# Optimization experiments

Measured on AMD Instinct MI355X. Metric: run time of the kernel, lower is better.

## Reference

```python
import jax, jax.numpy as jnp
import numpy as np

B, NQ, NKV, D, H = 8, 1024, 2048, 1024, 16
HD = D // H
EPS = 1e-5  # torch F.layer_norm default


def make_rope(n, hd):
    # standard RoPE tables: theta=10000, freqs repeated to head_dim via half/half layout
    inv = 1.0 / (10000.0 ** (np.arange(0, hd, 2, dtype=np.float64) / hd))
    ang = np.arange(n, dtype=np.float64)[:, None] * inv[None, :]  # [n, hd/2]
    ang = np.concatenate([ang, ang], axis=-1)  # [n, hd]
    return jnp.asarray(np.cos(ang), jnp.float32), jnp.asarray(np.sin(ang), jnp.float32)


def setup_inputs() -> dict:
    key = jax.random.key(0)
    ks = jax.random.split(key, 8)
    s = 1.0 / np.sqrt(D)
    q_cos, q_sin = make_rope(NQ, HD)
    kv_cos, kv_sin = make_rope(NKV, HD)
    return {
        "q_in": jax.random.normal(ks[0], (B, NQ, D), jnp.float32),
        "kv_in": jax.random.normal(ks[1], (B, NKV, D), jnp.float32),
        "q_cos": q_cos, "q_sin": q_sin,
        "kv_cos": kv_cos, "kv_sin": kv_sin,
        "Wq": jax.random.normal(ks[2], (D, D), jnp.float32) * s,
        "bq": jnp.zeros((D,), jnp.float32),
        "Wk": jax.random.normal(ks[3], (D, D), jnp.float32) * s,
        "bk": jnp.zeros((D,), jnp.float32),
        "Wv": jax.random.normal(ks[4], (D, D), jnp.float32) * s,
        "bv": jnp.zeros((D,), jnp.float32),
        "Wo": jax.random.normal(ks[5], (D, D), jnp.float32) * s,
        "bo": jnp.zeros((D,), jnp.float32),
    }


def _layer_norm(x):
    mu = jnp.mean(x, axis=-1, keepdims=True)
    var = jnp.mean(jnp.square(x - mu), axis=-1, keepdims=True)
    return (x - mu) * jax.lax.rsqrt(var + EPS)


def _to_multihead(x):
    # [B, N, D] -> [B, H, N, hd]
    b, n, _ = x.shape
    return x.reshape(b, n, H, HD).transpose(0, 2, 1, 3)


def _rotate_half(x):
    x1, x2 = jnp.split(x, 2, axis=-1)
    return jnp.concatenate([-x2, x1], axis=-1)


def _rope(x, cos, sin):
    # x: [B, H, N, hd]; cos/sin: [N, hd]
    return x * cos[None, None] + _rotate_half(x) * sin[None, None]


def reference(q_in, kv_in, q_cos, q_sin, kv_cos, kv_sin,
              Wq, bq, Wk, bk, Wv, bv, Wo, bo):
    qn = _layer_norm(q_in)
    kvn = _layer_norm(kv_in)
    q = _to_multihead(qn @ Wq.T + bq)
    k = _to_multihead(kvn @ Wk.T + bk)
    v = _to_multihead(kvn @ Wv.T + bv)
    q = _rope(q, q_cos, q_sin)
    k = _rope(k, kv_cos, kv_sin)
    # SDPA
    scores = jnp.einsum('bhqd,bhkd->bhqk', q, k) / np.sqrt(HD).astype(np.float32)
    attn = jax.nn.softmax(scores, axis=-1)
    out = jnp.einsum('bhqk,bhkd->bhqd', attn, v)  # [B, H, NQ, hd]
    out = out.transpose(0, 2, 1, 3).reshape(q_in.shape[0], q_in.shape[1], D)
    return out @ Wo.T + bo
```

## Files before the change

### kernel.cpp

```cpp
#include <hip/hip_runtime.h>
#include <stdint.h>
#include <stddef.h>

#define B_   8
#define NQ_  1024
#define NKV_ 2048
#define D_   1024
#define H_   16
#define HD_  64

typedef __bf16 bf16;
typedef __bf16 bf16x4 __attribute__((ext_vector_type(4)));
typedef __bf16 bf16x8 __attribute__((ext_vector_type(8)));
typedef float  f32x2  __attribute__((ext_vector_type(2)));
typedef float  f32x4  __attribute__((ext_vector_type(4)));
typedef float  f32x16 __attribute__((ext_vector_type(16)));
typedef unsigned int u32;
typedef u32 u32x2 __attribute__((ext_vector_type(2)));
typedef u32 u32x4 __attribute__((ext_vector_type(4)));
typedef unsigned short u16;

__device__ __forceinline__ void gload_lds16(const void* g, void* l) {
  __builtin_amdgcn_global_load_lds((const __attribute__((address_space(1))) void*)g,
                                   (__attribute__((address_space(3))) void*)l, 16, 0, 0);
}

__device__ __forceinline__ u32 pack2(float a, float b) {
  u16 ua = __builtin_bit_cast(u16, (bf16)a);
  u16 ub = __builtin_bit_cast(u16, (bf16)b);
  return (u32)ua | ((u32)ub << 16);
}

__global__ void cvt_w_kernel(const float* __restrict__ w0, const float* __restrict__ w1,
                             const float* __restrict__ w2, const float* __restrict__ w3,
                             bf16* __restrict__ o0, bf16* __restrict__ o1,
                             bf16* __restrict__ o2, bf16* __restrict__ o3) {
  const float* s; bf16* d;
  switch (blockIdx.y) {
    case 0: s = w0; d = o0; break;
    case 1: s = w1; d = o1; break;
    case 2: s = w2; d = o2; break;
    default: s = w3; d = o3; break;
  }
  int i = (blockIdx.x * 256 + threadIdx.x) * 4;
  float4 v = *(const float4*)(s + i);
  bf16x4 t = { (bf16)v.x, (bf16)v.y, (bf16)v.z, (bf16)v.w };
  *(bf16x4*)(d + i) = t;
}

__global__ void ln_bf16_kernel(const float* __restrict__ x, bf16* __restrict__ y) {
  int w = threadIdx.x >> 6, l = threadIdx.x & 63;
  int row = blockIdx.x * 4 + w;
  const float* xr = x + (size_t)row * D_;
  float4 v[4];
#pragma unroll
  for (int k = 0; k < 4; ++k) v[k] = *(const float4*)(xr + k * 256 + l * 4);
  float s = 0.f, ss = 0.f;
#pragma unroll
  for (int k = 0; k < 4; ++k) {
    s  += v[k].x + v[k].y + v[k].z + v[k].w;
    ss += v[k].x * v[k].x + v[k].y * v[k].y + v[k].z * v[k].z + v[k].w * v[k].w;
  }
#pragma unroll
  for (int m = 1; m < 64; m <<= 1) { s += __shfl_xor(s, m); ss += __shfl_xor(ss, m); }
  float mu = s * (1.f / D_);
  float var = ss * (1.f / D_) - mu * mu;
  float rs = rsqrtf(var + 1e-5f);
  bf16* yr = y + (size_t)row * D_;
#pragma unroll
  for (int k = 0; k < 4; ++k) {
    bf16x4 t = { (bf16)((v[k].x - mu) * rs), (bf16)((v[k].y - mu) * rs),
                 (bf16)((v[k].z - mu) * rs), (bf16)((v[k].w - mu) * rs) };
    *(bf16x4*)(yr + k * 256 + l * 4) = t;
  }
}

__device__ __forceinline__ int swz64(int row, int slot) {
  return row * 64 + ((slot ^ ((row >> 1) & 3)) << 4);
}

template<int EPI>
__global__ __launch_bounds__(256)
void gemm_bt(const bf16* __restrict__ A, const bf16* __restrict__ Bw,
             const float* __restrict__ bias,
             const float* __restrict__ cosT, const float* __restrict__ sinT,
             void* __restrict__ outp, int seq_shift) {
  __shared__ bf16 As[2][128 * 32];
  __shared__ bf16 Bs[2][128 * 32];
  const int tid = threadIdx.x;
  const int w = tid >> 6, l = tid & 63;
  const int wr = w >> 1, wc = w & 1;
  const int lg = l >> 4, lr = l & 15;
  const int mbase = blockIdx.y * 128, nbase = blockIdx.x * 128;

  f32x4 acc[4][4] = {};

  auto stage = [&](int k0, int buf) {
#pragma unroll
    for (int i = 0; i < 2; ++i) {
      int S = i * 256 + tid;
      int row = S >> 2, st = S & 3;
      int gs = st ^ ((row >> 1) & 3);
      gload_lds16((const char*)(A + ((size_t)(mbase + row) * 1024 + k0)) + gs * 16,
                  (char*)&As[buf][0] + (i * 256 + w * 64) * 16);
    }
#pragma unroll
    for (int i = 0; i < 2; ++i) {
      int S = i * 256 + tid;
      int row = S >> 2, st = S & 3;
      int gs = st ^ ((row >> 1) & 3);
      gload_lds16((const char*)(Bw + ((size_t)(nbase + row) * 1024 + k0)) + gs * 16,
                  (char*)&Bs[buf][0] + (i * 256 + w * 64) * 16);
    }
  };

  stage(0, 0);
  __syncthreads();
  for (int it = 0; it < 32; ++it) {
    int buf = it & 1;
    if (it + 1 < 32) stage((it + 1) * 32, buf ^ 1);
    bf16x8 af[4], bfr[4];
#pragma unroll
    for (int fr = 0; fr < 4; ++fr)
      af[fr] = *(const bf16x8*)((const char*)&As[buf][0] + swz64(wr * 64 + fr * 16 + lr, lg));
#pragma unroll
    for (int fc = 0; fc < 4; ++fc)
      bfr[fc] = *(const bf16x8*)((const char*)&Bs[buf][0] + swz64(wc * 64 + fc * 16 + lr, lg));
#pragma unroll
    for (int fr = 0; fr < 4; ++fr)
#pragma unroll
      for (int fc = 0; fc < 4; ++fc)
        acc[fr][fc] = __builtin_amdgcn_mfma_f32_16x16x32_bf16(af[fr], bfr[fc], acc[fr][fc], 0, 0, 0);
    __syncthreads();
  }

#pragma unroll
  for (int fr = 0; fr < 4; ++fr)
#pragma unroll
    for (int r = 0; r < 4; ++r) {
      int mrow = mbase + wr * 64 + fr * 16 + lg * 4 + r;
#pragma unroll
      for (int fc = 0; fc < 4; ++fc) {
        int n = nbase + wc * 64 + fc * 16 + lr;
        float x = acc[fr][fc][r];
        if (EPI == 0) {
          float xb  = x + bias[n];
          float xpb = acc[fr][fc ^ 2][r] + bias[n ^ 32];
          int d = n & 63, h = n >> 6;
          int seqN = 1 << seq_shift;
          int pos = mrow & (seqN - 1), bi = mrow >> seq_shift;
          float c = cosT[pos * 64 + d], s2 = sinT[pos * 64 + d];
          float yv = xb * c + ((d < 32) ? -xpb : xpb) * s2;
          ((bf16*)outp)[((size_t)(bi * H_ + h) * seqN + pos) * 64 + d] = (bf16)yv;
        } else if (EPI == 2) {
          int bi = n >> 11, kp = n & (NKV_ - 1);
          ((bf16*)outp)[(size_t)bi * (1024 * NKV_) + (size_t)mrow * NKV_ + kp] =
              (bf16)(x + bias[mrow]);
        } else {
          ((float*)outp)[(size_t)mrow * 1024 + n] = x + bias[n];
        }
      }
    }
}

__device__ __forceinline__ int swz128(int row, int slot) {
  return row * 128 + ((slot ^ (row & 7)) << 4);
}

__global__ __launch_bounds__(256)
void attn_kernel(const bf16* __restrict__ Qh, const bf16* __restrict__ Kh,
                 const bf16* __restrict__ Vt, bf16* __restrict__ Ao) {
  __shared__ bf16 Ks[2][64 * 64];
  __shared__ bf16 Vs[2][64 * 64];
  const int tid = threadIdx.x, wq = tid >> 6, l = tid & 63;
  const int q31 = l & 31, h = l >> 5;

  int bid = blockIdx.x;
  int vid = (bid & 7) * 128 + (bid >> 3);
  const int bh = vid >> 3;
  const int q0 = (vid & 7) * 128;

  bf16x8 aq[4];
  {
    const bf16* qrow = Qh + ((size_t)bh * NQ_ + q0 + wq * 32 + q31) * 64;
#pragma unroll
    for (int kt = 0; kt < 4; ++kt) aq[kt] = *(const bf16x8*)(qrow + kt * 16 + h * 8);
  }

  const char* Kbase = (const char*)(Kh + (size_t)bh * NKV_ * 64);
  const char* Vbase = (const char*)(Vt + (size_t)bh * 64 * NKV_);

  auto stageKV = [&](int t, int buf) {
#pragma unroll
    for (int i = 0; i < 2; ++i) {
      int S = i * 256 + tid;
      int row = S >> 3, st = S & 7;
      int gs = st ^ (row & 7);
      gload_lds16(Kbase + (size_t)(t * 64 + row) * 128 + gs * 16,
                  (char*)&Ks[buf][0] + (i * 256 + wq * 64) * 16);
    }
#pragma unroll
    for (int i = 0; i < 2; ++i) {
      int S = i * 256 + tid;
      int row = S >> 3, st = S & 7;
      int gs = st ^ (row & 7);
      gload_lds16(Vbase + (size_t)row * (NKV_ * 2) + (size_t)t * 128 + gs * 16,
                  (char*)&Vs[buf][0] + (i * 256 + wq * 64) * 16);
    }
  };

  float mrun = -3.0e38f, lrun = 0.f;
  f32x16 oaccT[2] = {};

  stageKV(0, 0);
  __syncthreads();

  const float SC = 0.125f * 1.44269504f;

  for (int t = 0; t < NKV_ / 64; ++t) {
    int buf = t & 1;
    if (t + 1 < NKV_ / 64) stageKV(t + 1, buf ^ 1);

    f32x16 st[2] = {};
    __builtin_amdgcn_s_setprio(1);
#pragma unroll
    for (int kvt = 0; kvt < 2; ++kvt)
#pragma unroll
      for (int kt = 0; kt < 4; ++kt) {
        bf16x8 kf = *(const bf16x8*)((const char*)&Ks[buf][0] +
                                     swz128(kvt * 32 + q31, kt * 2 + h));
        st[kvt] = __builtin_amdgcn_mfma_f32_32x32x16_bf16(kf, aq[kt], st[kvt], 0, 0, 0);
      }
    __builtin_amdgcn_s_setprio(0);

    f32x2 m2 = { -3.0e38f, -3.0e38f };
#pragma unroll
    for (int kvt = 0; kvt < 2; ++kvt)
#pragma unroll
      for (int i = 0; i < 8; ++i) {
        f32x2 v = { st[kvt][2 * i], st[kvt][2 * i + 1] };
        m2 = __builtin_elementwise_max(m2, v);
      }
    float ms = fmaxf(m2.x, m2.y);
    ms = fmaxf(ms, __shfl_xor(ms, 32));

    if (!__all((ms - mrun) * SC <= 8.0f)) {
      float mn = fmaxf(mrun, ms);
      float alpha = exp2f((mrun - mn) * SC);
      mrun = mn;
      lrun *= alpha;
#pragma unroll
      for (int dt = 0; dt < 2; ++dt) oaccT[dt] *= alpha;
    }
    float bterm = mrun * SC;

    f32x2 rs2 = { 0.f, 0.f };
    const f32x2 sc2 = { SC, SC };
    const f32x2 nb2 = { -bterm, -bterm };
#pragma unroll
    for (int kvt = 0; kvt < 2; ++kvt)
#pragma unroll
      for (int i = 0; i < 8; ++i) {
        f32x2 v = { st[kvt][2 * i], st[kvt][2 * i + 1] };
        v = v * sc2 + nb2;
        f32x2 p = { exp2f(v.x), exp2f(v.y) };
        st[kvt][2 * i] = p.x;
        st[kvt][2 * i + 1] = p.y;
        rs2 = rs2 + p;
      }
    float rs = rs2.x + rs2.y;
    rs += __shfl_xor(rs, 32);
    lrun += rs;

    bf16x8 pf[4];
#pragma unroll
    for (int kvt = 0; kvt < 2; ++kvt) {
      u32 E0 = pack2(st[kvt][0],  st[kvt][1]);
      u32 E1 = pack2(st[kvt][2],  st[kvt][3]);
      u32 O0 = pack2(st[kvt][4],  st[kvt][5]);
      u32 O1 = pack2(st[kvt][6],  st[kvt][7]);
      u32 E2 = pack2(st[kvt][8],  st[kvt][9]);
      u32 E3 = pack2(st[kvt][10], st[kvt][11]);
      u32 O2 = pack2(st[kvt][12], st[kvt][13]);
      u32 O3 = pack2(st[kvt][14], st[kvt][15]);
      u32 r0 = (u32)__shfl_xor((int)(h ? E0 : O0), 32);
      u32 r1 = (u32)__shfl_xor((int)(h ? E1 : O1), 32);
      u32 r2 = (u32)__shfl_xor((int)(h ? E2 : O2), 32);
      u32 r3 = (u32)__shfl_xor((int)(h ? E3 : O3), 32);
      u32x4 f0 = { h ? r0 : E0, h ? r1 : E1, h ? O0 : r0, h ? O1 : r1 };
      u32x4 f1 = { h ? r2 : E2, h ? r3 : E3, h ? O2 : r2, h ? O3 : r3 };
      pf[kvt * 2 + 0] = __builtin_bit_cast(bf16x8, f0);
      pf[kvt * 2 + 1] = __builtin_bit_cast(bf16x8, f1);
    }

    __builtin_amdgcn_s_setprio(1);
#pragma unroll
    for (int dt = 0; dt < 2; ++dt)
#pragma unroll
      for (int vt = 0; vt < 4; ++vt) {
        bf16x8 av = *(const bf16x8*)((const char*)&Vs[buf][0] +
                                     swz128(dt * 32 + q31, vt * 2 + h));
        oaccT[dt] = __builtin_amdgcn_mfma_f32_32x32x16_bf16(av, pf[vt], oaccT[dt], 0, 0, 0);
      }
    __builtin_amdgcn_s_setprio(0);
    __syncthreads();
  }

  float inv = 1.f / lrun;
  int b = bh >> 4, hh = bh & 15;
  bf16* orow = Ao + ((size_t)b * NQ_ + q0 + wq * 32 + q31) * D_ + hh * 64;
#pragma unroll
  for (int dt = 0; dt < 2; ++dt)
#pragma unroll
    for (int g = 0; g < 4; ++g) {
      int d = dt * 32 + 8 * g + 4 * h;
      u32 p0 = pack2(oaccT[dt][g * 4 + 0] * inv, oaccT[dt][g * 4 + 1] * inv);
      u32 p1 = pack2(oaccT[dt][g * 4 + 2] * inv, oaccT[dt][g * 4 + 3] * inv);
      *(u32*)(orow + d) = p0;
      *(u32*)(orow + d + 2) = p1;
    }
}

extern "C" void kernel_launch(void* const* d_in, const int* in_sizes, int n_in,
                              void* d_out, int out_size, void* d_ws, size_t ws_size,
                              hipStream_t stream) {
  (void)in_sizes; (void)n_in; (void)out_size; (void)ws_size;
  const float* q_in   = (const float*)d_in[0];
  const float* kv_in  = (const float*)d_in[1];
  const float* q_cos  = (const float*)d_in[2];
  const float* q_sin  = (const float*)d_in[3];
  const float* kv_cos = (const float*)d_in[4];
  const float* kv_sin = (const float*)d_in[5];
  const float* Wq = (const float*)d_in[6];
  const float* bq = (const float*)d_in[7];
  const float* Wk = (const float*)d_in[8];
  const float* bk = (const float*)d_in[9];
  const float* Wv = (const float*)d_in[10];
  const float* bv = (const float*)d_in[11];
  const float* Wo = (const float*)d_in[12];
  const float* bo = (const float*)d_in[13];

  char* ws = (char*)d_ws;
  bf16* qn  = (bf16*)ws;              ws += (size_t)B_ * NQ_ * D_ * 2;
  bf16* kvn = (bf16*)ws;              ws += (size_t)B_ * NKV_ * D_ * 2;
  bf16* wqb = (bf16*)ws;              ws += (size_t)D_ * D_ * 2;
  bf16* wkb = (bf16*)ws;              ws += (size_t)D_ * D_ * 2;
  bf16* wvb = (bf16*)ws;              ws += (size_t)D_ * D_ * 2;
  bf16* wob = (bf16*)ws;              ws += (size_t)D_ * D_ * 2;
  bf16* Qh  = (bf16*)ws;              ws += (size_t)B_ * H_ * NQ_ * 64 * 2;
  bf16* Kh  = (bf16*)ws;              ws += (size_t)B_ * H_ * NKV_ * 64 * 2;
  bf16* Vt  = (bf16*)ws;              ws += (size_t)B_ * H_ * 64 * NKV_ * 2;
  bf16* Ao  = qn;

  cvt_w_kernel<<<dim3(1024, 4), 256, 0, stream>>>(Wq, Wk, Wv, Wo, wqb, wkb, wvb, wob);
  ln_bf16_kernel<<<(B_ * NQ_) / 4, 256, 0, stream>>>(q_in, qn);
  ln_bf16_kernel<<<(B_ * NKV_) / 4, 256, 0, stream>>>(kv_in, kvn);

  gemm_bt<0><<<dim3(D_ / 128, (B_ * NQ_) / 128), 256, 0, stream>>>(
      qn, wqb, bq, q_cos, q_sin, (void*)Qh, 10);
  gemm_bt<0><<<dim3(D_ / 128, (B_ * NKV_) / 128), 256, 0, stream>>>(
      kvn, wkb, bk, kv_cos, kv_sin, (void*)Kh, 11);
  gemm_bt<2><<<dim3((B_ * NKV_) / 128, D_ / 128), 256, 0, stream>>>(
      wvb, kvn, bv, nullptr, nullptr, (void*)Vt, 0);

  attn_kernel<<<dim3((B_ * H_ * NQ_) / 128), 256, 0, stream>>>(Qh, Kh, Vt, Ao);

  gemm_bt<3><<<dim3(D_ / 128, (B_ * NQ_) / 128), 256, 0, stream>>>(
      Ao, wob, bo, nullptr, nullptr, d_out, 0);
}
```

Measured before the change: 576.1 us.

## Interleave RoPE tables, use hardware exp2/rcp, vectorize bf16 pack

Adds a kernel that interleaves the cos and sin tables into float2 pairs, so the RoPE epilogue of the QK projection does one 8-byte load per element instead of two scalar loads. The attention softmax now calls the raw hardware exp2 and reciprocal intrinsics instead of the libm-style exp2f and division. The bf16 pair packing uses a vector convert that can map to a packed conversion instruction. The cost is an extra small kernel launch plus workspace for the tables, and slightly reduced precision and denormal handling in exp2 and rcp.

```diff
diff --git a/kernel.cpp b/kernel.cpp
--- a/kernel.cpp
+++ b/kernel.cpp
@@ -10,6 +10,7 @@
 #define HD_  64
 
 typedef __bf16 bf16;
+typedef __bf16 bf16x2 __attribute__((ext_vector_type(2)));
 typedef __bf16 bf16x4 __attribute__((ext_vector_type(4)));
 typedef __bf16 bf16x8 __attribute__((ext_vector_type(8)));
 typedef float  f32x2  __attribute__((ext_vector_type(2)));
@@ -26,9 +27,8 @@
 }
 
 __device__ __forceinline__ u32 pack2(float a, float b) {
-  u16 ua = __builtin_bit_cast(u16, (bf16)a);
-  u16 ub = __builtin_bit_cast(u16, (bf16)b);
-  return (u32)ua | ((u32)ub << 16);
+  f32x2 v = { a, b };
+  return __builtin_bit_cast(u32, __builtin_convertvector(v, bf16x2));
 }
 
 __global__ void cvt_w_kernel(const float* __restrict__ w0, const float* __restrict__ w1,
@@ -48,6 +48,18 @@
   *(bf16x4*)(d + i) = t;
 }
 
+__global__ void build_cs_kernel(const float* __restrict__ qc, const float* __restrict__ qs,
+                                const float* __restrict__ kc, const float* __restrict__ ks,
+                                float2* __restrict__ qcs, float2* __restrict__ kcs) {
+  int i = blockIdx.x * 256 + threadIdx.x;
+  if (i < NQ_ * 64) {
+    qcs[i] = make_float2(qc[i], qs[i]);
+  } else {
+    int j = i - NQ_ * 64;
+    kcs[j] = make_float2(kc[j], ks[j]);
+  }
+}
+
 __global__ void ln_bf16_kernel(const float* __restrict__ x, bf16* __restrict__ y) {
   int w = threadIdx.x >> 6, l = threadIdx.x & 63;
   int row = blockIdx.x * 4 + w;
@@ -83,7 +95,7 @@
 __global__ __launch_bounds__(256)
 void gemm_bt(const bf16* __restrict__ A, const bf16* __restrict__ Bw,
              const float* __restrict__ bias,
-             const float* __restrict__ cosT, const float* __restrict__ sinT,
+             const float2* __restrict__ csT,
              void* __restrict__ outp, int seq_shift) {
   __shared__ bf16 As[2][128 * 32];
   __shared__ bf16 Bs[2][128 * 32];
@@ -149,8 +161,8 @@
           int d = n & 63, h = n >> 6;
           int seqN = 1 << seq_shift;
           int pos = mrow & (seqN - 1), bi = mrow >> seq_shift;
-          float c = cosT[pos * 64 + d], s2 = sinT[pos * 64 + d];
-          float yv = xb * c + ((d < 32) ? -xpb : xpb) * s2;
+          float2 cs = csT[pos * 64 + d];
+          float yv = xb * cs.x + ((d < 32) ? -xpb : xpb) * cs.y;
           ((bf16*)outp)[((size_t)(bi * H_ + h) * seqN + pos) * 64 + d] = (bf16)yv;
         } else if (EPI == 2) {
           int bi = n >> 11, kp = n & (NKV_ - 1);
@@ -246,7 +258,7 @@
 
     if (!__all((ms - mrun) * SC <= 8.0f)) {
       float mn = fmaxf(mrun, ms);
-      float alpha = exp2f((mrun - mn) * SC);
+      float alpha = __builtin_amdgcn_exp2f((mrun - mn) * SC);
       mrun = mn;
       lrun *= alpha;
 #pragma unroll
@@ -263,7 +275,7 @@
       for (int i = 0; i < 8; ++i) {
         f32x2 v = { st[kvt][2 * i], st[kvt][2 * i + 1] };
         v = v * sc2 + nb2;
-        f32x2 p = { exp2f(v.x), exp2f(v.y) };
+        f32x2 p = { __builtin_amdgcn_exp2f(v.x), __builtin_amdgcn_exp2f(v.y) };
         st[kvt][2 * i] = p.x;
         st[kvt][2 * i + 1] = p.y;
         rs2 = rs2 + p;
@@ -306,7 +318,7 @@
     __syncthreads();
   }
 
-  float inv = 1.f / lrun;
+  float inv = __builtin_amdgcn_rcpf(lrun);
   int b = bh >> 4, hh = bh & 15;
   bf16* orow = Ao + ((size_t)b * NQ_ + q0 + wq * 32 + q31) * D_ + hh * 64;
 #pragma unroll
@@ -350,21 +362,25 @@
   bf16* Qh  = (bf16*)ws;              ws += (size_t)B_ * H_ * NQ_ * 64 * 2;
   bf16* Kh  = (bf16*)ws;              ws += (size_t)B_ * H_ * NKV_ * 64 * 2;
   bf16* Vt  = (bf16*)ws;              ws += (size_t)B_ * H_ * 64 * NKV_ * 2;
+  float2* qcs = (float2*)ws;          ws += (size_t)NQ_ * 64 * sizeof(float2);
+  float2* kcs = (float2*)ws;          ws += (size_t)NKV_ * 64 * sizeof(float2);
   bf16* Ao  = qn;
 
   cvt_w_kernel<<<dim3(1024, 4), 256, 0, stream>>>(Wq, Wk, Wv, Wo, wqb, wkb, wvb, wob);
+  build_cs_kernel<<<(NQ_ * 64 + NKV_ * 64) / 256, 256, 0, stream>>>(
+      q_cos, q_sin, kv_cos, kv_sin, qcs, kcs);
   ln_bf16_kernel<<<(B_ * NQ_) / 4, 256, 0, stream>>>(q_in, qn);
   ln_bf16_kernel<<<(B_ * NKV_) / 4, 256, 0, stream>>>(kv_in, kvn);
 
   gemm_bt<0><<<dim3(D_ / 128, (B_ * NQ_) / 128), 256, 0, stream>>>(
-      qn, wqb, bq, q_cos, q_sin, (void*)Qh, 10);
+      qn, wqb, bq, qcs, (void*)Qh, 10);
   gemm_bt<0><<<dim3(D_ / 128, (B_ * NKV_) / 128), 256, 0, stream>>>(
-      kvn, wkb, bk, kv_cos, kv_sin, (void*)Kh, 11);
+      kvn, wkb, bk, kcs, (void*)Kh, 11);
   gemm_bt<2><<<dim3((B_ * NKV_) / 128, D_ / 128), 256, 0, stream>>>(
-      wvb, kvn, bv, nullptr, nullptr, (void*)Vt, 0);
+      wvb, kvn, bv, nullptr, (void*)Vt, 0);
 
   attn_kernel<<<dim3((B_ * H_ * NQ_) / 128), 256, 0, stream>>>(Qh, Kh, Vt, Ao);
 
   gemm_bt<3><<<dim3(D_ / 128, (B_ * NQ_) / 128), 256, 0, stream>>>(
-      Ao, wob, bo, nullptr, nullptr, d_out, 0);
-}
+      Ao, wob, bo, nullptr, d_out, 0);
+}
```

Result: faster. 524.2 us (-9.0%).
